# Kernel optimization log

Hardware: AMD Instinct MI355X
Metric: run time of the kernel (lower is better)

## Reference

```python
import jax, jax.numpy as jnp
import numpy as np

C = 256
C8 = C // 8

def setup_inputs() -> dict:
    key = jax.random.key(0)
    ks = jax.random.split(key, 8)
    a = jax.random.normal(ks[0], (4, C, 64, 64), dtype=jnp.float32)
    s = 1.0 / np.sqrt(C)
    b_w = jax.random.normal(ks[1], (C8, C), dtype=jnp.float32) * s
    b_b = jnp.zeros((C8,), dtype=jnp.float32)
    c_w = jax.random.normal(ks[2], (C8, C), dtype=jnp.float32) * s
    c_b = jnp.zeros((C8,), dtype=jnp.float32)
    d_w = jax.random.normal(ks[3], (C, C), dtype=jnp.float32) * s
    d_b = jnp.zeros((C,), dtype=jnp.float32)
    alpha = jnp.zeros((1,), dtype=jnp.float32) + 0.5  # nonzero so attention path is exercised
    return {"a": a, "b_w": b_w, "b_b": b_b, "c_w": c_w, "c_b": c_b, "d_w": d_w, "d_b": d_b, "alpha": alpha}

def _conv1x1(x, w, b):
    # x: [n, c, h, w], w: [o, c] -> [n, o, h, w]
    return jnp.einsum('nchw,oc->nohw', x, w) + b[None, :, None, None]

def reference(a, b_w, b_b, c_w, c_b, d_w, d_b, alpha):
    n, chan, h, w = a.shape
    nhw = h * w
    b = _conv1x1(a, b_w, b_b).reshape(n, -1, nhw)   # [n, C/8, nhw]
    c = _conv1x1(a, c_w, c_b).reshape(n, -1, nhw)   # [n, C/8, nhw]
    k = jnp.einsum('nci,ncj->nij', b, c)            # [n, nhw, nhw]
    s = jax.nn.softmax(k, axis=-1)
    d = _conv1x1(a, d_w, d_b).reshape(n, -1, nhw)   # [n, C, nhw]
    kl = jnp.einsum('ncj,nij->nci', d, s)           # d @ s^T
    kl = kl.reshape(n, chan, h, w)
    return alpha * kl + a
```

## Files before the change

### kernel.cpp

```cpp
#include <hip/hip_runtime.h>
#include <hip/hip_bf16.h>

#define CCH 256
#define CQK 32
#define NHW 4096

typedef float f32x4 __attribute__((ext_vector_type(4)));
typedef _Float16 hv8 __attribute__((ext_vector_type(8)));
typedef _Float16 hv4 __attribute__((ext_vector_type(4)));
typedef __fp16 fv2 __attribute__((ext_vector_type(2)));

typedef __attribute__((address_space(3))) unsigned int lds_u32_t;
typedef __attribute__((address_space(1))) const unsigned int glb_u32_t;
__device__ __forceinline__ void gll16(const _Float16* gp, _Float16* lp) {
    __builtin_amdgcn_global_load_lds((glb_u32_t*)gp, (lds_u32_t*)lp, 16, 0, 0);
}

__global__ __launch_bounds__(256) void prep_kernel(
    const float* __restrict__ b_w, const float* __restrict__ c_w,
    const float* __restrict__ d_w, _Float16* __restrict__ Wh)
{
    const int bid = blockIdx.x, tid = threadIdx.x;
    const int idx = (bid * 256 + tid) * 4;
    const int row = idx >> 8, col = idx & 255;
    const float* src = (row < 32) ? (b_w + row * CCH + col)
                     : (row < 64) ? (c_w + (row - 32) * CCH + col)
                                  : (d_w + (row - 64) * CCH + col);
    const float scl = (row < 32) ? 1.4426950408889634f : 1.0f;
    float4 v = *reinterpret_cast<const float4*>(src);
    _Float16* dst = Wh + (size_t)row * CCH + col;
    dst[0] = (_Float16)(v.x * scl); dst[1] = (_Float16)(v.y * scl);
    dst[2] = (_Float16)(v.z * scl); dst[3] = (_Float16)(v.w * scl);
}

__global__ __launch_bounds__(256) void proj_kernel(
    const float* __restrict__ a, const _Float16* __restrict__ Wh,
    const float* __restrict__ b_b, const float* __restrict__ c_b,
    const float* __restrict__ d_b,
    _Float16* __restrict__ bqT, _Float16* __restrict__ ckT,
    _Float16* __restrict__ dv)
{
    __shared__ _Float16 aT[32][CCH + 24];
    __shared__ _Float16 oT[256][34];
    __shared__ _Float16 pqT[32][34];
    __shared__ _Float16 pkT[32][34];

    const int n    = blockIdx.x >> 7;
    const int i0   = (blockIdx.x & 127) << 5;
    const int tid  = threadIdx.x;
    const int lane = tid & 63;
    const int wave = tid >> 6;
    const int l15  = lane & 15;
    const int quad = lane >> 4;

    {
        const float* ap = a + (size_t)(n*CCH + tid)*NHW + i0;
        #pragma unroll
        for (int j = 0; j < 8; ++j) {
            float4 v = *reinterpret_cast<const float4*>(ap + j*4);
            aT[j*4+0][tid] = (_Float16)v.x;
            aT[j*4+1][tid] = (_Float16)v.y;
            aT[j*4+2][tid] = (_Float16)v.z;
            aT[j*4+3][tid] = (_Float16)v.w;
        }
    }
    __syncthreads();

    const f32x4 zf = {0.f, 0.f, 0.f, 0.f};
    f32x4 acc[5][2];
    #pragma unroll
    for (int t = 0; t < 5; ++t) { acc[t][0] = zf; acc[t][1] = zf; }

    const int ch0w = wave * 80;

    #pragma unroll
    for (int ks = 0; ks < 8; ++ks) {
        const int k0 = ks * 32;
        hv8 af0 = *reinterpret_cast<const hv8*>(&aT[l15][k0 + quad*8]);
        hv8 af1 = *reinterpret_cast<const hv8*>(&aT[16 + l15][k0 + quad*8]);
        #pragma unroll
        for (int t = 0; t < 5; ++t) {
            const int ch0 = ch0w + t*16;
            hv8 bf = *reinterpret_cast<const hv8*>(
                Wh + (size_t)(ch0 + l15)*CCH + k0 + quad*8);
            acc[t][0] = __builtin_amdgcn_mfma_f32_16x16x32_f16(af0, bf, acc[t][0], 0, 0, 0);
            acc[t][1] = __builtin_amdgcn_mfma_f32_16x16x32_f16(af1, bf, acc[t][1], 0, 0, 0);
        }
    }

    const int posq = quad*4;
    #pragma unroll
    for (int t = 0; t < 5; ++t) {
        const int ch0 = ch0w + t*16;
        if (ch0 < 64) {
            const float* bias_arr = (ch0 < 32) ? b_b : c_b;
            const int    ch       = (ch0 & 31) + l15;
            const float  bias     = bias_arr[ch] *
                ((ch0 < 32) ? 1.4426950408889634f : 1.0f);
            #pragma unroll
            for (int nf = 0; nf < 2; ++nf) {
                #pragma unroll
                for (int r = 0; r < 4; ++r) {
                    const int pos = posq + nf*16 + r;
                    if (ch0 < 32) pqT[pos][ch] = (_Float16)(acc[t][nf][r] + bias);
                    else          pkT[pos][ch] = (_Float16)(acc[t][nf][r] + bias);
                }
            }
        } else {
            const int ch   = ch0 - 64 + l15;
            const float bias = d_b[ch];
            #pragma unroll
            for (int nf = 0; nf < 2; ++nf) {
                hv4 v = { (_Float16)(acc[t][nf][0] + bias),
                          (_Float16)(acc[t][nf][1] + bias),
                          (_Float16)(acc[t][nf][2] + bias),
                          (_Float16)(acc[t][nf][3] + bias) };
                *reinterpret_cast<hv4*>(&oT[ch][posq + nf*16]) = v;
            }
        }
    }
    __syncthreads();

    {
        const int p   = (tid & 127) >> 2;
        const int seg = (tid & 3) << 3;
        if (tid < 128) {
            *reinterpret_cast<int4*>(
                bqT + ((size_t)n*NHW + i0 + p)*CQK + seg) =
                *reinterpret_cast<const int4*>(&pqT[p][seg]);
        } else {
            *reinterpret_cast<int4*>(
                ckT + ((size_t)n*NHW + i0 + p)*CQK + seg) =
                *reinterpret_cast<const int4*>(&pkT[p][seg]);
        }
    }
    #pragma unroll
    for (int pass = 0; pass < 4; ++pass) {
        const int row = pass*64 + (tid >> 2);
        const int seg = (tid & 3) << 3;
        *reinterpret_cast<int4*>(
            dv + ((size_t)(n*CCH + row))*NHW + i0 + seg) =
            *reinterpret_cast<const int4*>(&oT[row][seg]);
    }
}

__global__ __launch_bounds__(512, 2) void attn_kernel(
    const _Float16* __restrict__ bqT, const _Float16* __restrict__ ckT,
    const _Float16* __restrict__ dv,
    const float* __restrict__ a, const float* __restrict__ alpha_p,
    float* __restrict__ out)
{
    __shared__ __align__(16) char smem[143360];

    const int bx   = ((blockIdx.x & 7) << 5) | (blockIdx.x >> 3);
    const int n    = bx >> 6;
    const int cg   = (bx >> 5) & 1;
    const int qt   = bx & 31;
    const int q0b  = qt << 7;
    const int co0  = cg << 7;
    const int tid  = threadIdx.x;
    const int wave = tid >> 6;
    const int g    = wave >> 1;
    const int qw   = wave & 1;
    const int lane = tid & 63;
    const int l15  = lane & 15;
    const int quad = lane >> 4;
    const int kg0  = g << 10;

    _Float16* vbuf = (_Float16*)(smem + (g << 14));
    _Float16* pb   = (_Float16*)(smem + 65536 + wave*9216);
    float*    lbuf = (float*)(smem + 139264);
    float*    mbuf = (float*)(smem + 141312);

    const f32x4 zf = {0.f, 0.f, 0.f, 0.f};
    const _Float16 one_h = (_Float16)1.0f;
    const hv8 ones = { one_h, one_h, one_h, one_h, one_h, one_h, one_h, one_h };

    hv8 qf[4];
    #pragma unroll
    for (int X = 0; X < 4; ++X) {
        const int q = q0b + qw*64 + X*16 + l15;
        qf[X] = *reinterpret_cast<const hv8*>(
            bqT + ((size_t)n*NHW + q)*CQK + quad*8);
    }

    const _Float16* ckbase = ckT + ((size_t)(n*NHW + kg0 + l15))*CQK + quad*8;

    float mneg[4] = {0.f, 0.f, 0.f, 0.f};

    f32x4 acc[4][8];
    #pragma unroll
    for (int X = 0; X < 4; ++X)
        #pragma unroll
        for (int t = 0; t < 8; ++t) acc[X][t] = zf;
    f32x4 accL[4];
    #pragma unroll
    for (int X = 0; X < 4; ++X) accL[X] = zf;

    const int rl8 = lane >> 3;
    const _Float16* dvs = dv
        + (size_t)(n*CCH + co0 + qw*64 + rl8)*NHW + kg0 + 8*((lane & 7) ^ rl8);
    _Float16* ldsb = (_Float16*)(smem + (g << 14) + qw*8192);

    const int c0h = ((quad*16) ^ ((l15 & 7) << 4)) >> 1;
    const int c1h = ((64 + quad*16) ^ ((l15 & 7) << 4)) >> 1;

    auto softmax_tile = [&](const hv8* kf) {
        #pragma unroll
        for (int X = 0; X < 4; ++X) {
            const f32x4 minit = {mneg[X], mneg[X], mneg[X], mneg[X]};
            f32x4 s0 = __builtin_amdgcn_mfma_f32_16x16x32_f16(kf[0], qf[X], minit, 0, 0, 0);
            f32x4 s1 = __builtin_amdgcn_mfma_f32_16x16x32_f16(kf[1], qf[X], minit, 0, 0, 0);
            f32x4 s2 = __builtin_amdgcn_mfma_f32_16x16x32_f16(kf[2], qf[X], minit, 0, 0, 0);
            f32x4 s3 = __builtin_amdgcn_mfma_f32_16x16x32_f16(kf[3], qf[X], minit, 0, 0, 0);
            float tm = fmaxf(
                fmaxf(fmaxf(fmaxf(s0[0], s0[1]), fmaxf(s0[2], s0[3])),
                      fmaxf(fmaxf(s1[0], s1[1]), fmaxf(s1[2], s1[3]))),
                fmaxf(fmaxf(fmaxf(s2[0], s2[1]), fmaxf(s2[2], s2[3])),
                      fmaxf(fmaxf(s3[0], s3[1]), fmaxf(s3[2], s3[3]))));
            tm = fmaxf(tm, __shfl_xor(tm, 16, 64));
            tm = fmaxf(tm, __shfl_xor(tm, 32, 64));
            const float upd = (tm > 8.0f) ? tm : 0.0f;
            if (__any(upd > 0.0f)) {
                const float sc = __builtin_amdgcn_exp2f(-upd);
                float s_r0 = __shfl(sc, quad*4 + 0, 64);
                float s_r1 = __shfl(sc, quad*4 + 1, 64);
                float s_r2 = __shfl(sc, quad*4 + 2, 64);
                float s_r3 = __shfl(sc, quad*4 + 3, 64);
                #pragma unroll
                for (int t = 0; t < 8; ++t) {
                    acc[X][t][0] *= s_r0; acc[X][t][1] *= s_r1;
                    acc[X][t][2] *= s_r2; acc[X][t][3] *= s_r3;
                }
                accL[X][0] *= s_r0; accL[X][1] *= s_r1;
                accL[X][2] *= s_r2; accL[X][3] *= s_r3;
                mneg[X] -= upd;
                s0[0] -= upd; s0[1] -= upd; s0[2] -= upd; s0[3] -= upd;
                s1[0] -= upd; s1[1] -= upd; s1[2] -= upd; s1[3] -= upd;
                s2[0] -= upd; s2[1] -= upd; s2[2] -= upd; s2[3] -= upd;
                s3[0] -= upd; s3[1] -= upd; s3[2] -= upd; s3[3] -= upd;
            }
            const f32x4 sv[4] = {s0, s1, s2, s3};
            #pragma unroll
            for (int f = 0; f < 4; ++f) {
                float p0 = __builtin_amdgcn_exp2f(sv[f][0]);
                float p1 = __builtin_amdgcn_exp2f(sv[f][1]);
                float p2 = __builtin_amdgcn_exp2f(sv[f][2]);
                float p3 = __builtin_amdgcn_exp2f(sv[f][3]);
                fv2 lo = __builtin_amdgcn_cvt_pkrtz(p0, p1);
                fv2 hi = __builtin_amdgcn_cvt_pkrtz(p2, p3);
                uint2 w;
                w.x = __builtin_bit_cast(unsigned, lo);
                w.y = __builtin_bit_cast(unsigned, hi);
                *reinterpret_cast<uint2*>(
                    pb + X*1152 + l15*72 + f*16 + quad*4) = w;
            }
        }
    };

    hv8 pf0[4], pf1[4];
    auto read_pf = [&]() {
        #pragma unroll
        for (int X = 0; X < 4; ++X) {
            pf0[X] = *reinterpret_cast<const hv8*>(pb + X*1152 + l15*72 + quad*8);
            pf1[X] = *reinterpret_cast<const hv8*>(pb + X*1152 + l15*72 + 32 + quad*8);
        }
    };

    auto stage = [&](int kt) {
        #pragma unroll
        for (int j = 0; j < 8; ++j)
            gll16(dvs + (size_t)(j*8)*NHW + kt*64, ldsb + (size_t)(j*8)*64);
    };

    auto load_kf = [&](int key0, hv8* kf) {
        #pragma unroll
        for (int f = 0; f < 4; ++f)
            kf[f] = *reinterpret_cast<const hv8*>(
                ckbase + (size_t)(key0 + f*16)*CQK);
    };

    {
        stage(0);
        hv8 kf0[4];
        load_kf(0, kf0);
        softmax_tile(kf0);
        read_pf();
    }
    __syncthreads();

    for (int kt = 0; kt < 16; ++kt) {
        hv8 kfn[4];
        if (kt < 15) load_kf((kt + 1)*64, kfn);

        #pragma unroll
        for (int t = 0; t < 8; ++t) {
            const _Float16* vr = vbuf + (t*16 + l15)*64;
            hv8 d0 = *reinterpret_cast<const hv8*>(vr + c0h);
            #pragma unroll
            for (int X = 0; X < 4; ++X)
                acc[X][t] = __builtin_amdgcn_mfma_f32_16x16x32_f16(
                    pf0[X], d0, acc[X][t], 0, 0, 0);
            hv8 d1 = *reinterpret_cast<const hv8*>(vr + c1h);
            #pragma unroll
            for (int X = 0; X < 4; ++X)
                acc[X][t] = __builtin_amdgcn_mfma_f32_16x16x32_f16(
                    pf1[X], d1, acc[X][t], 0, 0, 0);
        }
        #pragma unroll
        for (int X = 0; X < 4; ++X) {
            accL[X] = __builtin_amdgcn_mfma_f32_16x16x32_f16(pf0[X], ones, accL[X], 0, 0, 0);
            accL[X] = __builtin_amdgcn_mfma_f32_16x16x32_f16(pf1[X], ones, accL[X], 0, 0, 0);
        }

        if (kt < 15) {
            softmax_tile(kfn);
            __syncthreads();
            stage(kt + 1);
            read_pf();
            __syncthreads();
        }
    }

    if (lane < 16) {
        #pragma unroll
        for (int X = 0; X < 4; ++X)
            mbuf[g*128 + qw*64 + X*16 + l15] = -mneg[X];
    }
    __syncthreads();

    {
        #pragma unroll
        for (int X = 0; X < 4; ++X) {
            const int qloc = qw*64 + X*16 + quad*4;
            float4 m0 = *reinterpret_cast<float4*>(&mbuf[0*128 + qloc]);
            float4 m1 = *reinterpret_cast<float4*>(&mbuf[1*128 + qloc]);
            float4 m2 = *reinterpret_cast<float4*>(&mbuf[2*128 + qloc]);
            float4 m3 = *reinterpret_cast<float4*>(&mbuf[3*128 + qloc]);
            float4 mm;
            mm.x = fmaxf(fmaxf(m0.x, m1.x), fmaxf(m2.x, m3.x));
            mm.y = fmaxf(fmaxf(m0.y, m1.y), fmaxf(m2.y, m3.y));
            mm.z = fmaxf(fmaxf(m0.z, m1.z), fmaxf(m2.z, m3.z));
            mm.w = fmaxf(fmaxf(m0.w, m1.w), fmaxf(m2.w, m3.w));
            float4 mo = (g == 0) ? m0 : (g == 1) ? m1 : (g == 2) ? m2 : m3;
            float sc0 = __builtin_amdgcn_exp2f(mo.x - mm.x);
            float sc1 = __builtin_amdgcn_exp2f(mo.y - mm.y);
            float sc2 = __builtin_amdgcn_exp2f(mo.z - mm.z);
            float sc3 = __builtin_amdgcn_exp2f(mo.w - mm.w);
            #pragma unroll
            for (int t = 0; t < 8; ++t) {
                acc[X][t][0] *= sc0; acc[X][t][1] *= sc1;
                acc[X][t][2] *= sc2; acc[X][t][3] *= sc3;
            }
            accL[X][0] *= sc0; accL[X][1] *= sc1;
            accL[X][2] *= sc2; accL[X][3] *= sc3;
        }
    }

    float* buf1 = (float*)smem;
    float* buf2 = (float*)(smem + 67584);

    if (l15 == 0) {
        #pragma unroll
        for (int X = 0; X < 4; ++X)
            *reinterpret_cast<float4*>(&lbuf[g*128 + qw*64 + X*16 + quad*4]) =
                *reinterpret_cast<float4*>(&accL[X]);
    }
    if (g == 1 || g == 3) {
        float* b = (g == 1) ? buf1 : buf2;
        #pragma unroll
        for (int X = 0; X < 4; ++X)
            #pragma unroll
            for (int t = 0; t < 8; ++t)
                *reinterpret_cast<float4*>(
                    &b[(t*16 + l15)*132 + qw*64 + X*16 + quad*4]) =
                    *reinterpret_cast<float4*>(&acc[X][t]);
    }
    __syncthreads();
    if (g == 0 || g == 2) {
        float* b = (g == 0) ? buf1 : buf2;
        #pragma unroll
        for (int X = 0; X < 4; ++X)
            #pragma unroll
            for (int t = 0; t < 8; ++t) {
                float4 p = *reinterpret_cast<float4*>(
                    &b[(t*16 + l15)*132 + qw*64 + X*16 + quad*4]);
                acc[X][t][0] += p.x; acc[X][t][1] += p.y;
                acc[X][t][2] += p.z; acc[X][t][3] += p.w;
            }
    }
    __syncthreads();
    if (g == 2) {
        #pragma unroll
        for (int X = 0; X < 4; ++X)
            #pragma unroll
            for (int t = 0; t < 8; ++t)
                *reinterpret_cast<float4*>(
                    &buf1[(t*16 + l15)*132 + qw*64 + X*16 + quad*4]) =
                    *reinterpret_cast<float4*>(&acc[X][t]);
    }
    __syncthreads();
    if (g == 0) {
        const float alpha = alpha_p[0];
        #pragma unroll
        for (int X = 0; X < 4; ++X) {
            const int qlocX = qw*64 + X*16 + quad*4;
            #pragma unroll
            for (int t = 0; t < 8; ++t) {
                float4 p = *reinterpret_cast<float4*>(
                    &buf1[(t*16 + l15)*132 + qlocX]);
                acc[X][t][0] += p.x; acc[X][t][1] += p.y;
                acc[X][t][2] += p.z; acc[X][t][3] += p.w;
            }
            float4 l0 = *reinterpret_cast<float4*>(&lbuf[0*128 + qlocX]);
            float4 l1 = *reinterpret_cast<float4*>(&lbuf[1*128 + qlocX]);
            float4 l2 = *reinterpret_cast<float4*>(&lbuf[2*128 + qlocX]);
            float4 l3 = *reinterpret_cast<float4*>(&lbuf[3*128 + qlocX]);
            f32x4 rl;
            rl[0] = alpha / (l0.x + l1.x + l2.x + l3.x);
            rl[1] = alpha / (l0.y + l1.y + l2.y + l3.y);
            rl[2] = alpha / (l0.z + l1.z + l2.z + l3.z);
            rl[3] = alpha / (l0.w + l1.w + l2.w + l3.w);
            #pragma unroll
            for (int t = 0; t < 8; ++t) {
                const size_t off =
                    ((size_t)(n*CCH + co0 + t*16 + l15))*NHW + q0b + qlocX;
                float4 av = *reinterpret_cast<const float4*>(a + off);
                float4 o;
                o.x = acc[X][t][0]*rl[0] + av.x;
                o.y = acc[X][t][1]*rl[1] + av.y;
                o.z = acc[X][t][2]*rl[2] + av.z;
                o.w = acc[X][t][3]*rl[3] + av.w;
                *reinterpret_cast<float4*>(out + off) = o;
            }
        }
    }
}

extern "C" void kernel_launch(void* const* d_in, const int* in_sizes, int n_in,
                              void* d_out, int out_size, void* d_ws, size_t ws_size,
                              hipStream_t stream)
{
    const float* a    = (const float*)d_in[0];
    const float* b_w  = (const float*)d_in[1];
    const float* b_b  = (const float*)d_in[2];
    const float* c_w  = (const float*)d_in[3];
    const float* c_b  = (const float*)d_in[4];
    const float* d_w  = (const float*)d_in[5];
    const float* d_b  = (const float*)d_in[6];
    const float* alp  = (const float*)d_in[7];
    float* out = (float*)d_out;

    _Float16* bqT  = (_Float16*)d_ws;
    _Float16* ckT  = bqT + (size_t)4*NHW*CQK;
    _Float16* dv   = ckT + (size_t)4*NHW*CQK;
    _Float16* Wh   = dv + (size_t)4*CCH*NHW;

    prep_kernel<<<80, 256, 0, stream>>>(b_w, c_w, d_w, Wh);
    proj_kernel<<<512, 256, 0, stream>>>(a, Wh, b_b, c_b, d_b, bqT, ckT, dv);
    attn_kernel<<<256, 512, 0, stream>>>(bqT, ckT, dv, a, alp, out);
}
```

Measured before the change: 163.1 us.

## Precompute exact row max in a pre-pass, drop online softmax rescaling

Adds a pre-pass that computes the QK scores for every key in the block's key range and reduces them to each query row's maximum. The main loop then exponentiates with that fixed offset. This removes the per-tile max reduction, the cross-lane shuffles, the __any branch and the accumulator rescaling from the hot softmax loop. In exchange the QK MFMAs are recomputed and the K tiles are loaded from global memory a second time.

```diff
diff --git a/kernel.cpp b/kernel.cpp
--- a/kernel.cpp
+++ b/kernel.cpp
@@ -186,7 +186,37 @@
 
     const _Float16* ckbase = ckT + ((size_t)(n*NHW + kg0 + l15))*CQK + quad*8;
 
-    float mneg[4] = {0.f, 0.f, 0.f, 0.f};
+    float mneg[4];
+    {
+        float mx[4] = {-1e30f, -1e30f, -1e30f, -1e30f};
+        #pragma unroll
+        for (int bt = 0; bt < 8; ++bt) {
+            hv8 kb[8];
+            #pragma unroll
+            for (int j = 0; j < 8; ++j)
+                kb[j] = *reinterpret_cast<const hv8*>(
+                    ckbase + (size_t)(bt*128 + j*16)*CQK);
+            #pragma unroll
+            for (int X = 0; X < 4; ++X) {
+                float bm[8];
+                #pragma unroll
+                for (int j = 0; j < 8; ++j) {
+                    f32x4 s = __builtin_amdgcn_mfma_f32_16x16x32_f16(
+                        kb[j], qf[X], zf, 0, 0, 0);
+                    bm[j] = fmaxf(fmaxf(s[0], s[1]), fmaxf(s[2], s[3]));
+                }
+                float m0 = fmaxf(fmaxf(bm[0], bm[1]), fmaxf(bm[2], bm[3]));
+                float m1 = fmaxf(fmaxf(bm[4], bm[5]), fmaxf(bm[6], bm[7]));
+                mx[X] = fmaxf(mx[X], fmaxf(m0, m1));
+            }
+        }
+        #pragma unroll
+        for (int X = 0; X < 4; ++X) {
+            mx[X] = fmaxf(mx[X], __shfl_xor(mx[X], 16, 64));
+            mx[X] = fmaxf(mx[X], __shfl_xor(mx[X], 32, 64));
+            mneg[X] = -mx[X];
+        }
+    }
 
     f32x4 acc[4][8];
     #pragma unroll
@@ -209,44 +239,14 @@
         #pragma unroll
         for (int X = 0; X < 4; ++X) {
             const f32x4 minit = {mneg[X], mneg[X], mneg[X], mneg[X]};
-            f32x4 s0 = __builtin_amdgcn_mfma_f32_16x16x32_f16(kf[0], qf[X], minit, 0, 0, 0);
-            f32x4 s1 = __builtin_amdgcn_mfma_f32_16x16x32_f16(kf[1], qf[X], minit, 0, 0, 0);
-            f32x4 s2 = __builtin_amdgcn_mfma_f32_16x16x32_f16(kf[2], qf[X], minit, 0, 0, 0);
-            f32x4 s3 = __builtin_amdgcn_mfma_f32_16x16x32_f16(kf[3], qf[X], minit, 0, 0, 0);
-            float tm = fmaxf(
-                fmaxf(fmaxf(fmaxf(s0[0], s0[1]), fmaxf(s0[2], s0[3])),
-                      fmaxf(fmaxf(s1[0], s1[1]), fmaxf(s1[2], s1[3]))),
-                fmaxf(fmaxf(fmaxf(s2[0], s2[1]), fmaxf(s2[2], s2[3])),
-                      fmaxf(fmaxf(s3[0], s3[1]), fmaxf(s3[2], s3[3]))));
-            tm = fmaxf(tm, __shfl_xor(tm, 16, 64));
-            tm = fmaxf(tm, __shfl_xor(tm, 32, 64));
-            const float upd = (tm > 8.0f) ? tm : 0.0f;
-            if (__any(upd > 0.0f)) {
-                const float sc = __builtin_amdgcn_exp2f(-upd);
-                float s_r0 = __shfl(sc, quad*4 + 0, 64);
-                float s_r1 = __shfl(sc, quad*4 + 1, 64);
-                float s_r2 = __shfl(sc, quad*4 + 2, 64);
-                float s_r3 = __shfl(sc, quad*4 + 3, 64);
-                #pragma unroll
-                for (int t = 0; t < 8; ++t) {
-                    acc[X][t][0] *= s_r0; acc[X][t][1] *= s_r1;
-                    acc[X][t][2] *= s_r2; acc[X][t][3] *= s_r3;
-                }
-                accL[X][0] *= s_r0; accL[X][1] *= s_r1;
-                accL[X][2] *= s_r2; accL[X][3] *= s_r3;
-                mneg[X] -= upd;
-                s0[0] -= upd; s0[1] -= upd; s0[2] -= upd; s0[3] -= upd;
-                s1[0] -= upd; s1[1] -= upd; s1[2] -= upd; s1[3] -= upd;
-                s2[0] -= upd; s2[1] -= upd; s2[2] -= upd; s2[3] -= upd;
-                s3[0] -= upd; s3[1] -= upd; s3[2] -= upd; s3[3] -= upd;
-            }
-            const f32x4 sv[4] = {s0, s1, s2, s3};
             #pragma unroll
             for (int f = 0; f < 4; ++f) {
-                float p0 = __builtin_amdgcn_exp2f(sv[f][0]);
-                float p1 = __builtin_amdgcn_exp2f(sv[f][1]);
-                float p2 = __builtin_amdgcn_exp2f(sv[f][2]);
-                float p3 = __builtin_amdgcn_exp2f(sv[f][3]);
+                f32x4 s = __builtin_amdgcn_mfma_f32_16x16x32_f16(
+                    kf[f], qf[X], minit, 0, 0, 0);
+                float p0 = __builtin_amdgcn_exp2f(s[0]);
+                float p1 = __builtin_amdgcn_exp2f(s[1]);
+                float p2 = __builtin_amdgcn_exp2f(s[2]);
+                float p3 = __builtin_amdgcn_exp2f(s[3]);
                 fv2 lo = __builtin_amdgcn_cvt_pkrtz(p0, p1);
                 fv2 hi = __builtin_amdgcn_cvt_pkrtz(p2, p3);
                 uint2 w;
```

Result: no change. 164.6 us (+1.0%).
